# Performance work log

Measured on AMD Instinct MI355X. Metric: run time of the kernel, lower is better.

## Reference

```python
import jax, jax.numpy as jnp
import numpy as np

B, D, N = 256, 128, 65536
P, K, P2 = 100, 4096, 10
T, MOM = 0.07, 0.5


def setup_inputs() -> dict:
    key = jax.random.key(0)
    k1, k2, k3, k4, k5 = jax.random.split(key, 5)
    stdv = 1.0 / np.sqrt(D / 3.0)
    memory_v1 = jax.random.uniform(k1, (N, D), minval=-stdv, maxval=stdv, dtype=jnp.float32)
    memory_v2 = jax.random.uniform(k2, (N, D), minval=-stdv, maxval=stdv, dtype=jnp.float32)
    v1 = jax.random.normal(k3, (B, D), dtype=jnp.float32)
    v2 = jax.random.normal(k4, (B, D), dtype=jnp.float32)
    y = jnp.arange(B, dtype=jnp.int32)  # unique sample ids in the bank
    idx = jax.random.randint(k5, (B, K + P), 0, N, dtype=jnp.int32)
    idx = idx.at[:, 0].set(y)  # first column is the ground-truth positive (as in torch)
    return {"epoch": 0, "v1": v1, "v2": v2, "y": y, "idx": idx,
            "memory_v1": memory_v1, "memory_v2": memory_v2}


def reference(epoch, v1, v2, y, idx, memory_v1, memory_v2):
    # --- gather contrastive keys from the memory banks (detached in torch) ---
    w1 = jax.lax.stop_gradient(memory_v1)[idx]  # [B, K+P, D]
    w2 = jax.lax.stop_gradient(memory_v2)[idx]  # [B, K+P, D]

    # similarity logits against the student feature v2
    out = jnp.exp(jnp.einsum('bkd,bd->bk', w1, v2) / T)  # [B, K+P]

    # --- hard positive selection via teacher/student relation gap ---
    t_rel = jnp.einsum('bkd,bd->bk',
                       w1 / jnp.linalg.norm(w1, axis=2, keepdims=True),
                       v1 / jnp.linalg.norm(v1, axis=1, keepdims=True))
    s_rel = jnp.einsum('bkd,bd->bk',
                       w2 / jnp.linalg.norm(w2, axis=2, keepdims=True),
                       v2 / jnp.linalg.norm(v2, axis=1, keepdims=True))
    diff = t_rel[:, :P] - s_rel[:, :P]            # [B, P]
    order = jnp.argsort(-diff, axis=1)            # descending sort ('hard' mode)
    sel = order[:, :P2].at[:, 0].set(0)           # force slot 0 = ground-truth positive

    out_pos = jnp.take_along_axis(out, sel, axis=1)  # [B, P2]
    out_neg = out[:, P:P + K]                        # [B, K]
    out_cat = jnp.concatenate([out_pos, out_neg], axis=1)  # [B, P2+K]

    # normalization constant Z (first-iteration estimate; a detached scalar in torch)
    Z = jax.lax.stop_gradient(out_cat.mean() * N)
    out_final = (out_cat / Z)[:, :, None]  # [B, P2+K, 1]

    # --- momentum memory update (no_grad in torch) ---
    l = memory_v1[y] * MOM + v1 * (1.0 - MOM)
    new_mem_v1 = memory_v1.at[y].set(l / jnp.linalg.norm(l, axis=1, keepdims=True))
    new_mem_v1 = jax.lax.stop_gradient(new_mem_v1)
    # (memory_v2 is updated identically in torch but not returned; omitted from outputs)

    return out_final, new_mem_v1
```

## Files before the change

kernel.cpp:

```cpp
#include <hip/hip_runtime.h>
#include <math.h>

constexpr int B_ = 256;
constexpr int D_ = 128;
constexpr int N_ = 65536;
constexpr int P_ = 100;
constexpr int K_ = 4096;
constexpr int P2_ = 10;
constexpr int KP_ = K_ + P_;
constexpr int OC_ = P2_ + K_;
constexpr int NT_ = 512;
constexpr int SLOT_ = 2560;
constexpr float T_ = 0.07f;

typedef __attribute__((ext_vector_type(8))) short bf16x8;
typedef __attribute__((ext_vector_type(4))) float f32x4v;

__global__ __launch_bounds__(256) void k_prep(
    const float* __restrict__ v2, unsigned short* __restrict__ v2h,
    unsigned short* __restrict__ v2l, int* __restrict__ gcount)
{
  const int tid = threadIdx.x;
  if (blockIdx.x == 32) {
    gcount[tid] = 0;
    gcount[tid + 256] = 0;
    return;
  }
  const int i4 = blockIdx.x * 256 + tid;
  const float4 v = reinterpret_cast<const float4*>(v2)[i4];
  const float f[4] = {v.x, v.y, v.z, v.w};
  unsigned short h[4], l[4];
#pragma unroll
  for (int j = 0; j < 4; ++j) {
    const unsigned u = __float_as_uint(f[j]);
    h[j] = (unsigned short)(u >> 16);
    const float al = f[j] - __uint_as_float(u & 0xFFFF0000u);
    l[j] = (unsigned short)(__float_as_uint(al) >> 16);
  }
  ushort4 hv = {h[0], h[1], h[2], h[3]};
  ushort4 lv = {l[0], l[1], l[2], l[3]};
  reinterpret_cast<ushort4*>(v2h)[i4] = hv;
  reinterpret_cast<ushort4*>(v2l)[i4] = lv;
}

__global__ __launch_bounds__(256) void k_bin(
    const int* __restrict__ idx, unsigned* __restrict__ lists,
    int* __restrict__ gcount)
{
  const int b = blockIdx.x;
  const int tid = threadIdx.x;
  __shared__ int cnt[NT_];
  __shared__ int gbase[NT_];
  cnt[tid] = 0; cnt[tid + 256] = 0;
  __syncthreads();
  const int4* __restrict__ src = reinterpret_cast<const int4*>(idx + (size_t)b * KP_ + P_);
  unsigned short rows[16];
#pragma unroll
  for (int q = 0; q < 4; ++q) {
    const int4 r = src[q * 256 + tid];
    rows[q * 4 + 0] = (unsigned short)r.x;
    rows[q * 4 + 1] = (unsigned short)r.y;
    rows[q * 4 + 2] = (unsigned short)r.z;
    rows[q * 4 + 3] = (unsigned short)r.w;
    atomicAdd(&cnt[r.x >> 7], 1);
    atomicAdd(&cnt[r.y >> 7], 1);
    atomicAdd(&cnt[r.z >> 7], 1);
    atomicAdd(&cnt[r.w >> 7], 1);
  }
  __syncthreads();
  for (int t = tid; t < NT_; t += 256) {
    const int c = cnt[t];
    gbase[t] = c ? atomicAdd(&gcount[t], c) : 0;
  }
  __syncthreads();
  for (int t = tid; t < NT_; t += 256) cnt[t] = 0;
  __syncthreads();
#pragma unroll
  for (int q = 0; q < 4; ++q) {
#pragma unroll
    for (int u = 0; u < 4; ++u) {
      const int row = rows[q * 4 + u];
      const int tile = row >> 7;
      const int off = atomicAdd(&cnt[tile], 1);
      const int pos = gbase[tile] + off;
      if (pos < SLOT_)
        lists[(size_t)tile * SLOT_ + pos] =
            ((unsigned)(row & 127) << 20) | ((unsigned)b << 12) |
            (unsigned)((q * 256 + tid) * 4 + u);
    }
  }
}

__device__ inline void split8(const f32x4v lo, const f32x4v hi,
                              bf16x8& h, bf16x8& l) {
#pragma unroll
  for (int j = 0; j < 4; ++j) {
    const unsigned u = __float_as_uint(lo[j]);
    h[j] = (short)(u >> 16);
    const float al = lo[j] - __uint_as_float(u & 0xFFFF0000u);
    l[j] = (short)(__float_as_uint(al) >> 16);
  }
#pragma unroll
  for (int j = 0; j < 4; ++j) {
    const unsigned u = __float_as_uint(hi[j]);
    h[4 + j] = (short)(u >> 16);
    const float al = hi[j] - __uint_as_float(u & 0xFFFF0000u);
    l[4 + j] = (short)(__float_as_uint(al) >> 16);
  }
}

__global__ __launch_bounds__(512) void k_mega(
    const float* __restrict__ v1, const float* __restrict__ v2,
    const int* __restrict__ idx, const float* __restrict__ mem1,
    const float* __restrict__ mem2, const unsigned short* __restrict__ v2h,
    const unsigned short* __restrict__ v2l, const unsigned* __restrict__ lists,
    const int* __restrict__ gcount, float* __restrict__ out,
    float* __restrict__ outmem, double* __restrict__ wpart)
{
  const int tid = threadIdx.x;
  const unsigned bid = blockIdx.x;
  __shared__ char smem[66048];
  __shared__ double lacc8[8];
  __shared__ float sbuf[2 * D_];
  __shared__ double sdiff[P_];
  __shared__ float swout[P_];
  __shared__ double dsn2[P_], dss[P_];
  __shared__ double dinv[2];

  if (bid < 512) {
    const int r0 = bid * 128;
    {
      const float4* __restrict__ gsrc = reinterpret_cast<const float4*>(mem1 + (size_t)r0 * D_);
#pragma unroll
      for (int q = 0; q < 8; ++q) {
        const int li = q * 512 + tid;
        const float4 v = gsrc[li];
        const int row = li >> 5;
        const int off = (li & 31) * 16;
        *reinterpret_cast<float4*>(smem + row * 512 + (off ^ ((row & 7) << 4))) = v;
      }
    }
    __syncthreads();
    const int wid = tid >> 6, lane = tid & 63;
    const int mb = (wid >> 1) * 64;
    const int nb = (wid & 1) * 64;
    const int klane8 = (lane >> 4) * 8;
    f32x4v acc[4][4];
#pragma unroll
    for (int m = 0; m < 4; ++m)
#pragma unroll
      for (int n = 0; n < 4; ++n) acc[m][n] = {0.f, 0.f, 0.f, 0.f};

    const char* tb = (const char*)smem;
#pragma unroll
    for (int kk = 0; kk < 4; ++kk) {
      const int ks = kk * 32;
      bf16x8 ah[4], al[4];
#pragma unroll
      for (int m = 0; m < 4; ++m) {
        const size_t o = (size_t)(mb + m * 16 + (lane & 15)) * D_ + ks + klane8;
        ah[m] = *reinterpret_cast<const bf16x8*>(v2h + o);
        al[m] = *reinterpret_cast<const bf16x8*>(v2l + o);
      }
#pragma unroll
      for (int n = 0; n < 4; ++n) {
        const int r_loc = nb + n * 16 + (lane & 15);
        const int sw = (r_loc & 7) << 4;
        const int kb = (ks + klane8) * 4;
        const char* rb = tb + r_loc * 512;
        const f32x4v p0 = *reinterpret_cast<const f32x4v*>(rb + ((kb) ^ sw));
        const f32x4v p1 = *reinterpret_cast<const f32x4v*>(rb + ((kb + 16) ^ sw));
        bf16x8 bh, bl;
        split8(p0, p1, bh, bl);
#pragma unroll
        for (int m = 0; m < 4; ++m) {
          acc[m][n] = __builtin_amdgcn_mfma_f32_16x16x32_bf16(ah[m], bh, acc[m][n], 0, 0, 0);
          acc[m][n] = __builtin_amdgcn_mfma_f32_16x16x32_bf16(ah[m], bl, acc[m][n], 0, 0, 0);
          acc[m][n] = __builtin_amdgcn_mfma_f32_16x16x32_bf16(al[m], bh, acc[m][n], 0, 0, 0);
        }
      }
    }
    __syncthreads();
    float* eL = (float*)smem;
    const int tile = bid;
    const int cntT = min(gcount[tile], SLOT_);
    const unsigned* __restrict__ lb = lists + (size_t)tile * SLOT_;
    double de = 0.0;
#pragma unroll
    for (int half = 0; half < 2; ++half) {
      if ((mb < 128) == (half == 0)) {
#pragma unroll
        for (int m = 0; m < 4; ++m)
#pragma unroll
          for (int n = 0; n < 4; ++n) {
            const int rowloc = nb + n * 16 + (lane & 15);
            const int bloc = (mb & 64) + m * 16 + (lane >> 4) * 4;
#pragma unroll
            for (int reg = 0; reg < 4; ++reg)
              eL[rowloc * 129 + bloc + reg] = acc[m][n][reg];
          }
      }
      __syncthreads();
      for (int i = tid; i < cntT; i += 512) {
        const unsigned e = lb[i];
        const int bb = (e >> 12) & 255;
        if ((bb >> 7) == half) {
          const int rl = e >> 20;
          const int k = e & 4095;
          const float ex = expf(eL[rl * 129 + (bb & 127)] * (1.0f / T_));
          out[(size_t)bb * OC_ + P2_ + k] = ex;
          de += (double)ex;
        }
      }
      __syncthreads();
    }
#pragma unroll
    for (int sh = 1; sh < 64; sh <<= 1) de += __shfl_xor(de, sh);
    if ((tid & 63) == 0) lacc8[tid >> 6] = de;
    __syncthreads();
    if (tid == 0) {
      double s = 0.0;
#pragma unroll
      for (int w = 0; w < 8; ++w) s += lacc8[w];
      wpart[bid] = s;
    }
  } else if (bid < 768) {
    const int b = bid - 512;
    if (tid < 32)
      reinterpret_cast<float4*>(sbuf)[tid] =
          reinterpret_cast<const float4*>(v2 + (size_t)b * D_)[tid];
    else if (tid < 64)
      reinterpret_cast<float4*>(sbuf)[tid] =
          reinterpret_cast<const float4*>(v1 + (size_t)b * D_)[tid - 32];
    __syncthreads();
    if (tid < 64) {
      const float2* s2 = reinterpret_cast<const float2*>(sbuf);
      const float2 a = s2[tid];
      const float2 c = s2[64 + tid];
      double dn2 = (double)a.x * a.x + (double)a.y * a.y;
      double dn1 = (double)c.x * c.x + (double)c.y * c.y;
#pragma unroll
      for (int sh = 1; sh < 64; sh <<= 1) {
        dn2 += __shfl_xor(dn2, sh);
        dn1 += __shfl_xor(dn1, sh);
      }
      if (tid == 0) { dinv[0] = 1.0 / sqrt(dn1); dinv[1] = 1.0 / sqrt(dn2); }
    }
    if (tid >= 128 && tid < 128 + P_) {
      const int r = tid - 128;
      const int row = idx[(size_t)b * KP_ + r];
      const float4* __restrict__ w2p = reinterpret_cast<const float4*>(mem2 + (size_t)row * D_);
      const float4* __restrict__ x2p = reinterpret_cast<const float4*>(sbuf);
      double sn2 = 0, ss = 0;
#pragma unroll 4
      for (int jj = 0; jj < 32; ++jj) {
        const float4 cc = w2p[jj];
        const float4 y2 = x2p[jj];
        sn2 += (double)cc.x * cc.x + (double)cc.y * cc.y + (double)cc.z * cc.z + (double)cc.w * cc.w;
        ss  += (double)cc.x * y2.x + (double)cc.y * y2.y + (double)cc.z * y2.z + (double)cc.w * y2.w;
      }
      dsn2[r] = sn2; dss[r] = ss;
    }
    double so = 0, sn1 = 0, st = 0;
    if (tid < P_) {
      const int row = idx[(size_t)b * KP_ + tid];
      const float4* __restrict__ w1p = reinterpret_cast<const float4*>(mem1 + (size_t)row * D_);
      const float4* __restrict__ x2p = reinterpret_cast<const float4*>(sbuf);
      const float4* __restrict__ x1p = reinterpret_cast<const float4*>(sbuf + D_);
#pragma unroll 4
      for (int jj = 0; jj < 32; ++jj) {
        const float4 a  = w1p[jj];
        const float4 y1 = x1p[jj];
        const float4 y2 = x2p[jj];
        so  += (double)a.x * y2.x + (double)a.y * y2.y + (double)a.z * y2.z + (double)a.w * y2.w;
        sn1 += (double)a.x * a.x  + (double)a.y * a.y  + (double)a.z * a.z  + (double)a.w * a.w;
        st  += (double)a.x * y1.x + (double)a.y * y1.y + (double)a.z * y1.z + (double)a.w * y1.w;
      }
    }
    __syncthreads();
    if (tid < P_) {
      const double t_rel = st * dinv[0] / sqrt(sn1);
      const double s_rel = dss[tid] * dinv[1] / sqrt(dsn2[tid]);
      sdiff[tid] = t_rel - s_rel;
      swout[tid] = expf((float)(so * (1.0 / (double)T_)));
    }
    __syncthreads();
    if (tid < 64) {
      const int l = tid;
      const double va = sdiff[l];
      const double vb = (l < P_ - 64) ? sdiff[l + 64] : -1.0e300;
      bool ta = false, tb2 = (l >= P_ - 64);
      int sel[P2_];
#pragma unroll
      for (int t = 0; t < P2_; ++t) {
        double cv; int cj;
        const bool aok = !ta, bok = !tb2;
        if (aok && (!bok || va >= vb)) { cv = va; cj = l; }
        else if (bok)                  { cv = vb; cj = l + 64; }
        else                           { cv = -1.0e300; cj = 0x7fffffff; }
#pragma unroll
        for (int sh = 1; sh < 64; sh <<= 1) {
          const double ov = __shfl_xor(cv, sh);
          const int    oj = __shfl_xor(cj, sh);
          if (ov > cv || (ov == cv && oj < cj)) { cv = ov; cj = oj; }
        }
        sel[t] = cj;
        if (cj == l) ta = true;
        if (cj == l + 64) tb2 = true;
      }
      if (l == 0) {
        sel[0] = 0;
        double sp = 0.0;
#pragma unroll
        for (int t = 0; t < P2_; ++t) {
          const float e = swout[sel[t]];
          out[(size_t)b * OC_ + t] = e;
          sp += (double)e;
        }
        wpart[512 + b] = sp;
      }
    }
  } else {
    const int g = bid - 768;
    const float4* __restrict__ s4 = reinterpret_cast<const float4*>(mem1) + (size_t)g * 1024;
    float4* __restrict__ d4 = reinterpret_cast<float4*>(outmem) + (size_t)g * 1024;
    d4[tid] = s4[tid];
    d4[tid + 512] = s4[tid + 512];
  }
}

__global__ __launch_bounds__(256) void k_z(
    const double* __restrict__ wpart, float* __restrict__ invz)
{
  __shared__ double lds[4];
  const int tid = threadIdx.x;
  double s = 0.0;
  for (int i = tid; i < 768; i += 256) s += wpart[i];
#pragma unroll
  for (int sh = 1; sh < 64; sh <<= 1) s += __shfl_xor(s, sh);
  if ((tid & 63) == 0) lds[tid >> 6] = s;
  __syncthreads();
  if (tid == 0) {
    const double S = (lds[0] + lds[1]) + (lds[2] + lds[3]);
    const double Z = S / ((double)B_ * (double)OC_) * (double)N_;
    *invz = (float)(1.0 / Z);
  }
}

constexpr int NSC_ = (B_ * OC_ / 4 + 255) / 256;
__global__ __launch_bounds__(256) void k_scale_upd(
    float* __restrict__ out, const float* __restrict__ invz,
    const float* __restrict__ mem1, const float* __restrict__ v1,
    const int* __restrict__ y, float* __restrict__ dst)
{
  const int tid = threadIdx.x;
  if (blockIdx.x < NSC_) {
    const size_t i = (size_t)blockIdx.x * 256 + tid;
    constexpr size_t n4 = (size_t)B_ * OC_ / 4;
    if (i < n4) {
      const float sc = *invz;
      float4 v = reinterpret_cast<float4*>(out)[i];
      v.x *= sc; v.y *= sc; v.z *= sc; v.w *= sc;
      reinterpret_cast<float4*>(out)[i] = v;
    }
  } else if (tid < 64) {
    const int b = blockIdx.x - NSC_;
    const int row = y[b];
    const float2 m = *reinterpret_cast<const float2*>(mem1 + (size_t)row * D_ + tid * 2);
    const float2 a = *reinterpret_cast<const float2*>(v1 + (size_t)b * D_ + tid * 2);
    float2 l;
    l.x = m.x * 0.5f + a.x * 0.5f;
    l.y = m.y * 0.5f + a.y * 0.5f;
    float n = l.x * l.x + l.y * l.y;
#pragma unroll
    for (int sh = 1; sh < 64; sh <<= 1) n += __shfl_xor(n, sh);
    const float inv = 1.0f / sqrtf(n);
    float2 o;
    o.x = l.x * inv;
    o.y = l.y * inv;
    *reinterpret_cast<float2*>(dst + (size_t)row * D_ + tid * 2) = o;
  }
}

extern "C" void kernel_launch(void* const* d_in, const int* in_sizes, int n_in,
                              void* d_out, int out_size, void* d_ws, size_t ws_size,
                              hipStream_t stream) {
  const float* v1   = (const float*)d_in[1];
  const float* v2   = (const float*)d_in[2];
  const int*   y    = (const int*)d_in[3];
  const int*   idx  = (const int*)d_in[4];
  const float* mem1 = (const float*)d_in[5];
  const float* mem2 = (const float*)d_in[6];

  float* out    = (float*)d_out;
  float* outmem = out + (size_t)B_ * OC_;

  char* ws = (char*)d_ws;
  constexpr size_t LSZ = (size_t)NT_ * SLOT_ * 4;
  unsigned*       lists  = (unsigned*)ws;
  int*            gcount = (int*)(ws + LSZ);
  unsigned short* v2h    = (unsigned short*)(ws + LSZ + 4096);
  unsigned short* v2l    = (unsigned short*)(ws + LSZ + 4096 + 65536);
  double*         wpart  = (double*)(ws + LSZ + 4096 + 2 * 65536);
  float*          invz   = (float*)(ws + LSZ + 4096 + 2 * 65536 + 8192);

  k_prep<<<33, 256, 0, stream>>>(v2, v2h, v2l, gcount);
  k_bin<<<B_, 256, 0, stream>>>(idx, lists, gcount);
  k_mega<<<2816, 512, 0, stream>>>(v1, v2, idx, mem1, mem2, v2h, v2l,
                                   lists, gcount, out, outmem, wpart);
  k_z<<<1, 256, 0, stream>>>(wpart, invz);
  k_scale_upd<<<NSC_ + B_, 256, 0, stream>>>(out, invz, mem1, v1, y, outmem);
}
```

Baseline: 77.47 us.

## Halve GEMM tile to 64 rows, load B directly from global, reorder block roles

The memory-bank GEMM tile shrinks from 128 to 64 rows, giving 1024 tiles with smaller per-tile lists. B operands are now read straight from global memory instead of being staged in shared memory, and the two-pass half-split epilogue becomes a single pass over a 64x257 LDS layout. Cosine/selection blocks are moved to the front of the grid, and launch bounds now request 4 blocks per CU. The aim is more parallelism, better tail balance and less shared-memory staging and sync, at the cost of more list and gcount traffic and uncoalesced global B loads.

Result: slower. 91.07 us (+17.6%).

```diff
diff --git a/kernel.cpp b/kernel.cpp
--- a/kernel.cpp
+++ b/kernel.cpp
@@ -9,8 +9,11 @@
 constexpr int P2_ = 10;
 constexpr int KP_ = K_ + P_;
 constexpr int OC_ = P2_ + K_;
-constexpr int NT_ = 512;
-constexpr int SLOT_ = 2560;
+constexpr int NT_ = 1024;
+constexpr int SLOT_ = 1536;
+constexpr int GCOS_ = 256;
+constexpr int GGEMM_ = 1024;
+constexpr int GCOPY_ = 2048;
 constexpr float T_ = 0.07f;
 
 typedef __attribute__((ext_vector_type(8))) short bf16x8;
@@ -24,6 +27,8 @@
   if (blockIdx.x == 32) {
     gcount[tid] = 0;
     gcount[tid + 256] = 0;
+    gcount[tid + 512] = 0;
+    gcount[tid + 768] = 0;
     return;
   }
   const int i4 = blockIdx.x * 256 + tid;
@@ -51,7 +56,7 @@
   const int tid = threadIdx.x;
   __shared__ int cnt[NT_];
   __shared__ int gbase[NT_];
-  cnt[tid] = 0; cnt[tid + 256] = 0;
+  for (int t = tid; t < NT_; t += 256) cnt[t] = 0;
   __syncthreads();
   const int4* __restrict__ src = reinterpret_cast<const int4*>(idx + (size_t)b * KP_ + P_);
   unsigned short rows[16];
@@ -62,10 +67,10 @@
     rows[q * 4 + 1] = (unsigned short)r.y;
     rows[q * 4 + 2] = (unsigned short)r.z;
     rows[q * 4 + 3] = (unsigned short)r.w;
-    atomicAdd(&cnt[r.x >> 7], 1);
-    atomicAdd(&cnt[r.y >> 7], 1);
-    atomicAdd(&cnt[r.z >> 7], 1);
-    atomicAdd(&cnt[r.w >> 7], 1);
+    atomicAdd(&cnt[r.x >> 6], 1);
+    atomicAdd(&cnt[r.y >> 6], 1);
+    atomicAdd(&cnt[r.z >> 6], 1);
+    atomicAdd(&cnt[r.w >> 6], 1);
   }
   __syncthreads();
   for (int t = tid; t < NT_; t += 256) {
@@ -80,12 +85,12 @@
 #pragma unroll
     for (int u = 0; u < 4; ++u) {
       const int row = rows[q * 4 + u];
-      const int tile = row >> 7;
+      const int tile = row >> 6;
       const int off = atomicAdd(&cnt[tile], 1);
       const int pos = gbase[tile] + off;
       if (pos < SLOT_)
         lists[(size_t)tile * SLOT_ + pos] =
-            ((unsigned)(row & 127) << 20) | ((unsigned)b << 12) |
+            ((unsigned)(row & 63) << 20) | ((unsigned)b << 12) |
             (unsigned)((q * 256 + tid) * 4 + u);
     }
   }
@@ -109,7 +114,7 @@
   }
 }
 
-__global__ __launch_bounds__(512) void k_mega(
+__global__ __launch_bounds__(512, 4) void k_mega(
     const float* __restrict__ v1, const float* __restrict__ v2,
     const int* __restrict__ idx, const float* __restrict__ mem1,
     const float* __restrict__ mem2, const unsigned short* __restrict__ v2h,
@@ -119,113 +124,17 @@
 {
   const int tid = threadIdx.x;
   const unsigned bid = blockIdx.x;
-  __shared__ char smem[66048];
+  __shared__ char smem[65792];
   __shared__ double lacc8[8];
-  __shared__ float sbuf[2 * D_];
-  __shared__ double sdiff[P_];
-  __shared__ float swout[P_];
-  __shared__ double dsn2[P_], dss[P_];
-  __shared__ double dinv[2];
-
-  if (bid < 512) {
-    const int r0 = bid * 128;
-    {
-      const float4* __restrict__ gsrc = reinterpret_cast<const float4*>(mem1 + (size_t)r0 * D_);
-#pragma unroll
-      for (int q = 0; q < 8; ++q) {
-        const int li = q * 512 + tid;
-        const float4 v = gsrc[li];
-        const int row = li >> 5;
-        const int off = (li & 31) * 16;
-        *reinterpret_cast<float4*>(smem + row * 512 + (off ^ ((row & 7) << 4))) = v;
-      }
-    }
-    __syncthreads();
-    const int wid = tid >> 6, lane = tid & 63;
-    const int mb = (wid >> 1) * 64;
-    const int nb = (wid & 1) * 64;
-    const int klane8 = (lane >> 4) * 8;
-    f32x4v acc[4][4];
-#pragma unroll
-    for (int m = 0; m < 4; ++m)
-#pragma unroll
-      for (int n = 0; n < 4; ++n) acc[m][n] = {0.f, 0.f, 0.f, 0.f};
-
-    const char* tb = (const char*)smem;
-#pragma unroll
-    for (int kk = 0; kk < 4; ++kk) {
-      const int ks = kk * 32;
-      bf16x8 ah[4], al[4];
-#pragma unroll
-      for (int m = 0; m < 4; ++m) {
-        const size_t o = (size_t)(mb + m * 16 + (lane & 15)) * D_ + ks + klane8;
-        ah[m] = *reinterpret_cast<const bf16x8*>(v2h + o);
-        al[m] = *reinterpret_cast<const bf16x8*>(v2l + o);
-      }
-#pragma unroll
-      for (int n = 0; n < 4; ++n) {
-        const int r_loc = nb + n * 16 + (lane & 15);
-        const int sw = (r_loc & 7) << 4;
-        const int kb = (ks + klane8) * 4;
-        const char* rb = tb + r_loc * 512;
-        const f32x4v p0 = *reinterpret_cast<const f32x4v*>(rb + ((kb) ^ sw));
-        const f32x4v p1 = *reinterpret_cast<const f32x4v*>(rb + ((kb + 16) ^ sw));
-        bf16x8 bh, bl;
-        split8(p0, p1, bh, bl);
-#pragma unroll
-        for (int m = 0; m < 4; ++m) {
-          acc[m][n] = __builtin_amdgcn_mfma_f32_16x16x32_bf16(ah[m], bh, acc[m][n], 0, 0, 0);
-          acc[m][n] = __builtin_amdgcn_mfma_f32_16x16x32_bf16(ah[m], bl, acc[m][n], 0, 0, 0);
-          acc[m][n] = __builtin_amdgcn_mfma_f32_16x16x32_bf16(al[m], bh, acc[m][n], 0, 0, 0);
-        }
-      }
-    }
-    __syncthreads();
-    float* eL = (float*)smem;
-    const int tile = bid;
-    const int cntT = min(gcount[tile], SLOT_);
-    const unsigned* __restrict__ lb = lists + (size_t)tile * SLOT_;
-    double de = 0.0;
-#pragma unroll
-    for (int half = 0; half < 2; ++half) {
-      if ((mb < 128) == (half == 0)) {
-#pragma unroll
-        for (int m = 0; m < 4; ++m)
-#pragma unroll
-          for (int n = 0; n < 4; ++n) {
-            const int rowloc = nb + n * 16 + (lane & 15);
-            const int bloc = (mb & 64) + m * 16 + (lane >> 4) * 4;
-#pragma unroll
-            for (int reg = 0; reg < 4; ++reg)
-              eL[rowloc * 129 + bloc + reg] = acc[m][n][reg];
-          }
-      }
-      __syncthreads();
-      for (int i = tid; i < cntT; i += 512) {
-        const unsigned e = lb[i];
-        const int bb = (e >> 12) & 255;
-        if ((bb >> 7) == half) {
-          const int rl = e >> 20;
-          const int k = e & 4095;
-          const float ex = expf(eL[rl * 129 + (bb & 127)] * (1.0f / T_));
-          out[(size_t)bb * OC_ + P2_ + k] = ex;
-          de += (double)ex;
-        }
-      }
-      __syncthreads();
-    }
-#pragma unroll
-    for (int sh = 1; sh < 64; sh <<= 1) de += __shfl_xor(de, sh);
-    if ((tid & 63) == 0) lacc8[tid >> 6] = de;
-    __syncthreads();
-    if (tid == 0) {
-      double s = 0.0;
-#pragma unroll
-      for (int w = 0; w < 8; ++w) s += lacc8[w];
-      wpart[bid] = s;
-    }
-  } else if (bid < 768) {
-    const int b = bid - 512;
+
+  if (bid < GCOS_) {
+    float* sbuf = (float*)smem;
+    double* sdiff = (double*)(smem + 1024);
+    float* swout = (float*)(smem + 1024 + 800);
+    double* dsn2 = (double*)(smem + 1024 + 800 + 416);
+    double* dss = (double*)(smem + 1024 + 800 + 416 + 800);
+    double* dinv = (double*)(smem + 1024 + 800 + 416 + 1600);
+    const int b = bid;
     if (tid < 32)
       reinterpret_cast<float4*>(sbuf)[tid] =
           reinterpret_cast<const float4*>(v2 + (size_t)b * D_)[tid];
@@ -317,11 +226,84 @@
           out[(size_t)b * OC_ + t] = e;
           sp += (double)e;
         }
-        wpart[512 + b] = sp;
-      }
+        wpart[GGEMM_ + b] = sp;
+      }
+    }
+  } else if (bid < GCOS_ + GGEMM_) {
+    const int tile = bid - GCOS_;
+    const int r0 = tile * 64;
+    const int wid = tid >> 6, lane = tid & 63;
+    const int mb = (wid >> 1) * 64;
+    const int nb = (wid & 1) * 32;
+    const int klane8 = (lane >> 4) * 8;
+    f32x4v acc[4][2];
+#pragma unroll
+    for (int m = 0; m < 4; ++m)
+#pragma unroll
+      for (int n = 0; n < 2; ++n) acc[m][n] = {0.f, 0.f, 0.f, 0.f};
+
+#pragma unroll
+    for (int kk = 0; kk < 4; ++kk) {
+      const int ks = kk * 32;
+      bf16x8 ah[4], al[4];
+#pragma unroll
+      for (int m = 0; m < 4; ++m) {
+        const size_t o = (size_t)(mb + m * 16 + (lane & 15)) * D_ + ks + klane8;
+        ah[m] = *reinterpret_cast<const bf16x8*>(v2h + o);
+        al[m] = *reinterpret_cast<const bf16x8*>(v2l + o);
+      }
+#pragma unroll
+      for (int n = 0; n < 2; ++n) {
+        const int row = r0 + nb + n * 16 + (lane & 15);
+        const float* __restrict__ bp = mem1 + (size_t)row * D_ + ks + klane8;
+        const f32x4v p0 = *reinterpret_cast<const f32x4v*>(bp);
+        const f32x4v p1 = *reinterpret_cast<const f32x4v*>(bp + 4);
+        bf16x8 bh, bl;
+        split8(p0, p1, bh, bl);
+#pragma unroll
+        for (int m = 0; m < 4; ++m) {
+          acc[m][n] = __builtin_amdgcn_mfma_f32_16x16x32_bf16(ah[m], bh, acc[m][n], 0, 0, 0);
+          acc[m][n] = __builtin_amdgcn_mfma_f32_16x16x32_bf16(ah[m], bl, acc[m][n], 0, 0, 0);
+          acc[m][n] = __builtin_amdgcn_mfma_f32_16x16x32_bf16(al[m], bh, acc[m][n], 0, 0, 0);
+        }
+      }
+    }
+    float* eL = (float*)smem;
+#pragma unroll
+    for (int m = 0; m < 4; ++m)
+#pragma unroll
+      for (int n = 0; n < 2; ++n) {
+        const int rowloc = nb + n * 16 + (lane & 15);
+        const int bloc = mb + m * 16 + (lane >> 4) * 4;
+#pragma unroll
+        for (int reg = 0; reg < 4; ++reg)
+          eL[rowloc * 257 + bloc + reg] = acc[m][n][reg];
+      }
+    __syncthreads();
+    const int cntT = min(gcount[tile], SLOT_);
+    const unsigned* __restrict__ lb = lists + (size_t)tile * SLOT_;
+    double de = 0.0;
+    for (int i = tid; i < cntT; i += 512) {
+      const unsigned e = lb[i];
+      const int rl = e >> 20;
+      const int bb = (e >> 12) & 255;
+      const int k = e & 4095;
+      const float ex = expf(eL[rl * 257 + bb] * (1.0f / T_));
+      out[(size_t)bb * OC_ + P2_ + k] = ex;
+      de += (double)ex;
+    }
+#pragma unroll
+    for (int sh = 1; sh < 64; sh <<= 1) de += __shfl_xor(de, sh);
+    if (lane == 0) lacc8[wid] = de;
+    __syncthreads();
+    if (tid == 0) {
+      double s = 0.0;
+#pragma unroll
+      for (int w = 0; w < 8; ++w) s += lacc8[w];
+      wpart[tile] = s;
     }
   } else {
-    const int g = bid - 768;
+    const int g = bid - GCOS_ - GGEMM_;
     const float4* __restrict__ s4 = reinterpret_cast<const float4*>(mem1) + (size_t)g * 1024;
     float4* __restrict__ d4 = reinterpret_cast<float4*>(outmem) + (size_t)g * 1024;
     d4[tid] = s4[tid];
@@ -335,7 +317,7 @@
   __shared__ double lds[4];
   const int tid = threadIdx.x;
   double s = 0.0;
-  for (int i = tid; i < 768; i += 256) s += wpart[i];
+  for (int i = tid; i < GGEMM_ + B_; i += 256) s += wpart[i];
 #pragma unroll
   for (int sh = 1; sh < 64; sh <<= 1) s += __shfl_xor(s, sh);
   if ((tid & 63) == 0) lds[tid >> 6] = s;
@@ -399,15 +381,15 @@
   constexpr size_t LSZ = (size_t)NT_ * SLOT_ * 4;
   unsigned*       lists  = (unsigned*)ws;
   int*            gcount = (int*)(ws + LSZ);
-  unsigned short* v2h    = (unsigned short*)(ws + LSZ + 4096);
-  unsigned short* v2l    = (unsigned short*)(ws + LSZ + 4096 + 65536);
-  double*         wpart  = (double*)(ws + LSZ + 4096 + 2 * 65536);
-  float*          invz   = (float*)(ws + LSZ + 4096 + 2 * 65536 + 8192);
+  unsigned short* v2h    = (unsigned short*)(ws + LSZ + 8192);
+  unsigned short* v2l    = (unsigned short*)(ws + LSZ + 8192 + 65536);
+  double*         wpart  = (double*)(ws + LSZ + 8192 + 2 * 65536);
+  float*          invz   = (float*)(ws + LSZ + 8192 + 2 * 65536 + 16384);
 
   k_prep<<<33, 256, 0, stream>>>(v2, v2h, v2l, gcount);
   k_bin<<<B_, 256, 0, stream>>>(idx, lists, gcount);
-  k_mega<<<2816, 512, 0, stream>>>(v1, v2, idx, mem1, mem2, v2h, v2l,
-                                   lists, gcount, out, outmem, wpart);
+  k_mega<<<GCOS_ + GGEMM_ + GCOPY_, 512, 0, stream>>>(
+      v1, v2, idx, mem1, mem2, v2h, v2l, lists, gcount, out, outmem, wpart);
   k_z<<<1, 256, 0, stream>>>(wpart, invz);
   k_scale_upd<<<NSC_ + B_, 256, 0, stream>>>(out, invz, mem1, v1, y, outmem);
 }
```
